# Kernel tuning notes

Hardware: AMD Instinct MI355X
Metric: run time of the kernel (lower is better)

Reference implementation:

```python
import jax, jax.numpy as jnp
import numpy as np

B, S, E = 1024, 128, 256   # batch, num fields, embed size
H, D = 8, 64               # head_num, att_embed_size
SCALING = False


def setup_inputs() -> dict:
    key = jax.random.key(0)
    k0, k1, k2, k3, k4 = jax.random.split(key, 5)
    return {
        "inputs": jax.random.normal(k0, (B, S, E), dtype=jnp.float32),
        "w_query": jax.random.truncated_normal(k1, -2.0, 2.0, (E, H * D), dtype=jnp.float32) * 0.05,
        "w_key": jax.random.truncated_normal(k2, -2.0, 2.0, (E, H * D), dtype=jnp.float32) * 0.05,
        "w_value": jax.random.truncated_normal(k3, -2.0, 2.0, (E, H * D), dtype=jnp.float32) * 0.05,
        "w_res": jax.random.truncated_normal(k4, -2.0, 2.0, (E, H * D), dtype=jnp.float32) * 0.05,
    }


def reference(inputs, w_query, w_key, w_value, w_res):
    b, s, _ = inputs.shape
    # QKV projections, split into heads: tf.split on last dim == reshape (b,s,H,D)
    q = (inputs @ w_query).reshape(b, s, H, D)
    k = (inputs @ w_key).reshape(b, s, H, D)
    v = (inputs @ w_value).reshape(b, s, H, D)
    scores = jnp.einsum("bqhd,bkhd->bhqk", q, k)
    if SCALING:
        scores = scores / jnp.sqrt(jnp.float32(D))
    att = jax.nn.softmax(scores, axis=-1)
    out = jnp.einsum("bhqk,bkhd->bqhd", att, v).reshape(b, s, H * D)
    out = out + inputs @ w_res  # residual projection (use_res=True)
    return jax.nn.relu(out)
```

## Files before the change

kernel.cpp:

```cpp
#include <hip/hip_runtime.h>

#define B_ 1024
#define S_ 128
#define E_ 256
#define H_ 8
#define D_ 64
#define HD_ 512

typedef short s16x8 __attribute__((ext_vector_type(8)));
typedef float f32x4 __attribute__((ext_vector_type(4)));
typedef unsigned int u32x4 __attribute__((ext_vector_type(4)));
typedef unsigned short u16;
typedef unsigned int u32;

struct U16x8 { u16 v[8]; };

__device__ __forceinline__ u16 f2bf(float f) {
  u32 u = __float_as_uint(f);
  u += 0x7FFFu + ((u >> 16) & 1u);
  return (u16)(u >> 16);
}

__device__ __forceinline__ u32 cvtpk_bf16(float lo, float hi) {
  u32 r;
  asm("v_cvt_pk_bf16_f32 %0, %1, %2" : "=v"(r) : "v"(lo), "v"(hi));
  return r;
}

__device__ __forceinline__ void dma_w(const u16* __restrict__ WF, int base8,
                                      u16* dst, int tid) {
  const char* g = (const char*)WF + (size_t)base8 * 32768 + (size_t)tid * 16;
  char* l = (char*)dst + tid * 16;
#pragma unroll
  for (int j = 0; j < 4; ++j)
    __builtin_amdgcn_global_load_lds(
        (const __attribute__((address_space(1))) void*)(g + j * 8192),
        (__attribute__((address_space(3))) void*)(l + j * 8192), 16, 0, 0);
}

__global__ __launch_bounds__(256) void probe_dtype(const u32* __restrict__ x,
                                                   u32* __restrict__ flag) {
  __shared__ int cnt;
  if (threadIdx.x == 0) cnt = 0;
  __syncthreads();
  u32 w = x[threadIdx.x];
  u32 e = (w >> 7) & 0xFFu;
  if (e > 96u && e < 160u) atomicAdd(&cnt, 1);
  __syncthreads();
  if (threadIdx.x == 0) flag[0] = (cnt > 128) ? 1u : 0u;
}

__global__ __launch_bounds__(256) void repack_w(
    const void* __restrict__ wqv, const void* __restrict__ wkv,
    const void* __restrict__ wvv, const void* __restrict__ wrv,
    const u32* __restrict__ flag, u16* __restrict__ wf) {
  bool isbf = (flag[0] != 0u);
  int t = blockIdx.x * 256 + threadIdx.x;
  int lane = t & 63;
  int tc   = (t >> 6) & 3;
  int ks   = (t >> 8) & 7;
  int h    = (t >> 11) & 7;
  int w    = (t >> 14) & 3;
  const void* srcv = (w == 0) ? wqv : (w == 1) ? wkv : (w == 2) ? wvv : wrv;
  int n  = h * D_ + tc * 16 + (lane & 15);
  int e0 = ks * 32 + (lane >> 4) * 8;
  U16x8 tmp;
  if (isbf) {
    const u16* s = (const u16*)srcv;
#pragma unroll
    for (int j = 0; j < 8; ++j) tmp.v[j] = s[(e0 + j) * HD_ + n];
  } else {
    const float* s = (const float*)srcv;
#pragma unroll
    for (int j = 0; j < 8; ++j) tmp.v[j] = f2bf(s[(e0 + j) * HD_ + n]);
  }
  *(u32x4*)(wf + (size_t)t * 8) = *(const u32x4*)tmp.v;
}

__device__ __forceinline__ void proj4_lds(const u16* __restrict__ Wb, int lane,
                                          const s16x8 xfrag[8], f32x4 acc[4]) {
  const u32x4* w4 = (const u32x4*)Wb + lane;
#pragma unroll
  for (int tc = 0; tc < 4; ++tc) acc[tc] = (f32x4){0.f, 0.f, 0.f, 0.f};
#pragma unroll
  for (int ks = 0; ks < 8; ++ks) {
#pragma unroll
    for (int tc = 0; tc < 4; ++tc) {
      u32x4 raw = w4[(ks * 4 + tc) * 64];
      s16x8 bfr = *(const s16x8*)&raw;
      acc[tc] = __builtin_amdgcn_mfma_f32_16x16x32_bf16(xfrag[ks], bfr, acc[tc], 0, 0, 0);
    }
  }
}

__device__ __forceinline__ void proj4_direct(const void* __restrict__ srcv, bool isbf,
                                             int h, int lane, const s16x8 xfrag[8],
                                             f32x4 acc[4]) {
#pragma unroll
  for (int tc = 0; tc < 4; ++tc) acc[tc] = (f32x4){0.f, 0.f, 0.f, 0.f};
  int e8 = (lane >> 4) * 8;
  int nc = h * D_ + (lane & 15);
#pragma unroll
  for (int ks = 0; ks < 8; ++ks) {
#pragma unroll
    for (int tc = 0; tc < 4; ++tc) {
      U16x8 tmp;
      if (isbf) {
        const u16* s = (const u16*)srcv;
#pragma unroll
        for (int j = 0; j < 8; ++j) tmp.v[j] = s[(ks * 32 + e8 + j) * HD_ + nc + tc * 16];
      } else {
        const float* s = (const float*)srcv;
#pragma unroll
        for (int j = 0; j < 8; ++j) tmp.v[j] = f2bf(s[(ks * 32 + e8 + j) * HD_ + nc + tc * 16]);
      }
      s16x8 bfr = *(const s16x8*)tmp.v;
      acc[tc] = __builtin_amdgcn_mfma_f32_16x16x32_bf16(xfrag[ks], bfr, acc[tc], 0, 0, 0);
    }
  }
}

__device__ __forceinline__ void scatter_qk(u16* dst, int w, int quad, int col,
                                           const f32x4 acc[4]) {
#pragma unroll
  for (int tc = 0; tc < 4; ++tc) {
    int ks2 = tc >> 1;
    int q2  = (tc & 1) * 2 + (col >> 3);
#pragma unroll
    for (int r = 0; r < 4; ++r)
      dst[(((w * 2 + ks2) * 64) + q2 * 16 + quad * 4 + r) * 8 + (col & 7)] =
          f2bf(acc[tc][r]);
  }
}

__device__ __forceinline__ void scatter_v(u16* Vf, int w, int quad, int col,
                                          const f32x4 acc[4]) {
#pragma unroll
  for (int tc = 0; tc < 4; ++tc)
#pragma unroll
    for (int r = 0; r < 4; ++r) {
      int srow = quad * 4 + r;
      int q2   = (w & 1) * 2 + (srow >> 3);
      Vf[((((w >> 1) * 4 + tc) * 64) + q2 * 16 + col) * 8 + (srow & 7)] =
          f2bf(acc[tc][r]);
    }
}

__global__ __launch_bounds__(512) void mha_fused(
    const void* __restrict__ Xv, const u16* __restrict__ WF,
    const void* __restrict__ wqv, const void* __restrict__ wkv,
    const void* __restrict__ wvv, const void* __restrict__ wrv,
    void* __restrict__ outv, const u32* __restrict__ flag, int useWF) {
  __shared__ __align__(16) u16 smem[73728];
  u16* Wb0 = smem;
  u16* Wb1 = smem + 16384;
  u16* Qf  = smem + 32768;
  u16* KfB = smem + 40960;
  u16* VfB = smem + 57344;

  const bool isbf = (flag[0] != 0u);
  const int tid  = threadIdx.x;
  const int w    = tid >> 6;
  const int lane = tid & 63;
  const int quad = lane >> 4;
  const int col  = lane & 15;
  const int b    = blockIdx.x;

  if (useWF) dma_w(WF, 0, Wb0, tid);

  s16x8 xfrag[8];
  {
    u32x4* xs = (u32x4*)KfB;
#pragma unroll
    for (int half = 0; half < 2; ++half) {
      int cbase = half * 2048;
#pragma unroll
      for (int k = 0; k < 4; ++k) {
        int c  = cbase + tid + k * 512;
        int s  = c >> 5;
        int e0 = (c & 31) * 8;
        U16x8 tmp;
        if (isbf) {
          const u32x4* xg = (const u32x4*)Xv + (size_t)b * 4096;
          u32x4 raw = xg[c];
          tmp = *(const U16x8*)&raw;
        } else {
          const f32x4* xg = (const f32x4*)Xv + (size_t)b * 8192;
          f32x4 lo = xg[2 * c], hi = xg[2 * c + 1];
#pragma unroll
          for (int j = 0; j < 4; ++j) { tmp.v[j] = f2bf(lo[j]); tmp.v[4 + j] = f2bf(hi[j]); }
        }
        xs[(((s >> 4) & 3) * 8 + (e0 >> 5)) * 64 + ((e0 >> 3) & 3) * 16 + (s & 15)] =
            *(const u32x4*)tmp.v;
      }
      __syncthreads();
      if ((w >> 2) == half) {
        int trl = w & 3;
#pragma unroll
        for (int ks = 0; ks < 8; ++ks) {
          u32x4 raw = xs[(trl * 8 + ks) * 64 + lane];
          xfrag[ks] = *(const s16x8*)&raw;
        }
      }
      __syncthreads();
    }
  }

  s16x8 aq[2];
  f32x4 ra[4];

  const int sl0 = (lane & 15) | ((lane & 16) << 1);
  const bool hiq = (lane >= 32);

  for (int h = 0; h <= H_; ++h) {
    const int hp = h - 1;
    const u16* Kp = KfB + (hp & 1) * 8192;
    const u16* Vp = VfB + (hp & 1) * 8192;
    u16* Kc = KfB + (h & 1) * 8192;
    u16* Vc = VfB + (h & 1) * 8192;

    f32x4 sacc[8];
    u32 wp[8][2];
    f32x4 oacc[4];
    float linv = 0.f;
    s16x8 aqn[2];
    f32x4 acc[4];

    __syncthreads();
    if (useWF && h < H_) dma_w(WF, 8 + h, Wb1, tid);
    if (h < H_) {
      if (useWF) proj4_lds(Wb0, lane, xfrag, acc);
      else       proj4_direct(wqv, isbf, h, lane, xfrag, acc);
      scatter_qk(Qf, w, quad, col, acc);
      aqn[0] = *(const s16x8*)(Qf + ((w * 2 + 0) * 64 + lane) * 8);
      aqn[1] = *(const s16x8*)(Qf + ((w * 2 + 1) * 64 + lane) * 8);
    }
    if (h > 0) {
#pragma unroll
      for (int tS = 0; tS < 8; ++tS) {
        sacc[tS] = (f32x4){0.f, 0.f, 0.f, 0.f};
#pragma unroll
        for (int k2 = 0; k2 < 2; ++k2) {
          s16x8 bk = *(const s16x8*)(Kp + ((tS * 2 + k2) * 64 + lane) * 8);
          sacc[tS] = __builtin_amdgcn_mfma_f32_16x16x32_bf16(bk, aq[k2], sacc[tS], 0, 0, 0);
        }
      }
    }
    if (h < H_) { aq[0] = aqn[0]; aq[1] = aqn[1]; }

    __syncthreads();
    if (useWF && h < H_) dma_w(WF, 16 + h, Wb0, tid);
    if (h < H_) {
      if (useWF) proj4_lds(Wb1, lane, xfrag, acc);
      else       proj4_direct(wkv, isbf, h, lane, xfrag, acc);
      scatter_qk(Kc, w, quad, col, acc);
    }
    if (h > 0) {
      float m = sacc[0][0];
#pragma unroll
      for (int tS = 0; tS < 8; ++tS)
#pragma unroll
        for (int r = 0; r < 4; ++r) m = fmaxf(m, sacc[tS][r]);
      m = fmaxf(m, __shfl_xor(m, 16));
      m = fmaxf(m, __shfl_xor(m, 32));
      float lsum = 0.f;
#pragma unroll
      for (int tS = 0; tS < 8; ++tS)
#pragma unroll
        for (int r = 0; r < 4; ++r) {
          float e = __expf(sacc[tS][r] - m);
          sacc[tS][r] = e;
          lsum += e;
        }
      lsum += __shfl_xor(lsum, 16);
      lsum += __shfl_xor(lsum, 32);
      linv = 1.0f / lsum;
#pragma unroll
      for (int tS = 0; tS < 8; ++tS) {
        wp[tS][0] = cvtpk_bf16(sacc[tS][0], sacc[tS][1]);
        wp[tS][1] = cvtpk_bf16(sacc[tS][2], sacc[tS][3]);
      }
    }

    __syncthreads();
    if (useWF && h < H_) dma_w(WF, 24 + h, Wb1, tid);
    if (h < H_) {
      if (useWF) proj4_lds(Wb0, lane, xfrag, acc);
      else       proj4_direct(wvv, isbf, h, lane, xfrag, acc);
      scatter_v(Vc, w, quad, col, acc);
    }
    if (h > 0) {
#pragma unroll
      for (int tc = 0; tc < 4; ++tc) oacc[tc] = (f32x4){0.f, 0.f, 0.f, 0.f};
#pragma unroll
      for (int kt = 0; kt < 4; ++kt) {
        int a00 = __shfl((int)wp[2 * kt][0],     sl0);
        int a01 = __shfl((int)wp[2 * kt][1],     sl0);
        int a10 = __shfl((int)wp[2 * kt + 1][0], sl0);
        int a11 = __shfl((int)wp[2 * kt + 1][1], sl0);
        int b00 = __shfl((int)wp[2 * kt][0],     sl0 + 16);
        int b01 = __shfl((int)wp[2 * kt][1],     sl0 + 16);
        int b10 = __shfl((int)wp[2 * kt + 1][0], sl0 + 16);
        int b11 = __shfl((int)wp[2 * kt + 1][1], sl0 + 16);
        u32x4 av;
        av[0] = (u32)(hiq ? a10 : a00);
        av[1] = (u32)(hiq ? a11 : a01);
        av[2] = (u32)(hiq ? b10 : b00);
        av[3] = (u32)(hiq ? b11 : b01);
        s16x8 ap = *(const s16x8*)&av;
#pragma unroll
        for (int tc = 0; tc < 4; ++tc) {
          s16x8 bv = *(const s16x8*)(Vp + ((kt * 4 + tc) * 64 + lane) * 8);
          oacc[tc] = __builtin_amdgcn_mfma_f32_16x16x32_bf16(ap, bv, oacc[tc], 0, 0, 0);
        }
      }
    }

    __syncthreads();
    if (useWF && h + 1 < H_) dma_w(WF, h + 1, Wb0, tid);
    if (h < H_) {
      if (useWF) proj4_lds(Wb1, lane, xfrag, acc);
      else       proj4_direct(wrv, isbf, h, lane, xfrag, acc);
    }
    if (h > 0) {
      float linv_e[4];
#pragma unroll
      for (int r = 0; r < 4; ++r) linv_e[r] = __shfl(linv, quad * 4 + r);
#pragma unroll
      for (int tc = 0; tc < 4; ++tc)
#pragma unroll
        for (int r = 0; r < 4; ++r) {
          float v = oacc[tc][r] * linv_e[r] + ra[tc][r];
          v = fmaxf(v, 0.f);
          int s = w * 16 + quad * 4 + r;
          size_t idx = ((size_t)b * S_ + s) * HD_ + hp * D_ + tc * 16 + col;
          if (isbf) ((u16*)outv)[idx] = f2bf(v);
          else      ((float*)outv)[idx] = v;
        }
    }
    if (h < H_) {
#pragma unroll
      for (int tc = 0; tc < 4; ++tc) ra[tc] = acc[tc];
    }
  }
}

extern "C" void kernel_launch(void* const* d_in, const int* in_sizes, int n_in,
                              void* d_out, int out_size, void* d_ws, size_t ws_size,
                              hipStream_t stream) {
  const void* X  = d_in[0];
  const void* wq = d_in[1];
  const void* wk = d_in[2];
  const void* wv = d_in[3];
  const void* wr = d_in[4];

  u32* flag = (u32*)d_ws;
  u16* wf   = (u16*)((char*)d_ws + 4096);
  int useWF = (ws_size >= (size_t)(1u << 20) + 4096) ? 1 : 0;

  probe_dtype<<<dim3(1), dim3(256), 0, stream>>>((const u32*)X, flag);
  if (useWF)
    repack_w<<<dim3(256), dim3(256), 0, stream>>>(wq, wk, wv, wr, flag, wf);
  mha_fused<<<dim3(B_), dim3(512), 0, stream>>>(X, wf, wq, wk, wv, wr, d_out, flag, useWF);
}
```

Baseline: 579.6 us.

## Process two batch elements per block to share staged weight tiles

Each block now handles two batch elements, so every weight tile copied into LDS feeds twice as many MFMAs, and the grid is halved. The head loop is rescheduled: the second batch's PV and epilogue are deferred to the next iteration, and the K/V buffers are split per batch instead of ping-ponged per head. The aim is to halve weight traffic into LDS and the per-block setup cost. In exchange, register pressure rises (two X fragment sets and two accumulator sets), which may cause spills. With fewer, longer blocks there is also less latitude to balance load across CUs.

```diff
diff --git a/kernel.cpp b/kernel.cpp
--- a/kernel.cpp
+++ b/kernel.cpp
@@ -77,18 +77,23 @@
   *(u32x4*)(wf + (size_t)t * 8) = *(const u32x4*)tmp.v;
 }
 
-__device__ __forceinline__ void proj4_lds(const u16* __restrict__ Wb, int lane,
-                                          const s16x8 xfrag[8], f32x4 acc[4]) {
+__device__ __forceinline__ void proj4_lds2(const u16* __restrict__ Wb, int lane,
+                                           const s16x8 xf0[8], const s16x8 xf1[8],
+                                           f32x4 a0[4], f32x4 a1[4]) {
   const u32x4* w4 = (const u32x4*)Wb + lane;
 #pragma unroll
-  for (int tc = 0; tc < 4; ++tc) acc[tc] = (f32x4){0.f, 0.f, 0.f, 0.f};
+  for (int tc = 0; tc < 4; ++tc) {
+    a0[tc] = (f32x4){0.f, 0.f, 0.f, 0.f};
+    a1[tc] = (f32x4){0.f, 0.f, 0.f, 0.f};
+  }
 #pragma unroll
   for (int ks = 0; ks < 8; ++ks) {
 #pragma unroll
     for (int tc = 0; tc < 4; ++tc) {
       u32x4 raw = w4[(ks * 4 + tc) * 64];
       s16x8 bfr = *(const s16x8*)&raw;
-      acc[tc] = __builtin_amdgcn_mfma_f32_16x16x32_bf16(xfrag[ks], bfr, acc[tc], 0, 0, 0);
+      a0[tc] = __builtin_amdgcn_mfma_f32_16x16x32_bf16(xf0[ks], bfr, a0[tc], 0, 0, 0);
+      a1[tc] = __builtin_amdgcn_mfma_f32_16x16x32_bf16(xf1[ks], bfr, a1[tc], 0, 0, 0);
     }
   }
 }
@@ -144,6 +149,129 @@
       Vf[((((w >> 1) * 4 + tc) * 64) + q2 * 16 + col) * 8 + (srow & 7)] =
           f2bf(acc[tc][r]);
     }
+}
+
+__device__ __forceinline__ void qk_sm(const u16* __restrict__ Kp, const s16x8 aqb[2],
+                                      int lane, u32 wp[8][2], float& linv) {
+  f32x4 sacc[8];
+#pragma unroll
+  for (int tS = 0; tS < 8; ++tS) {
+    sacc[tS] = (f32x4){0.f, 0.f, 0.f, 0.f};
+#pragma unroll
+    for (int k2 = 0; k2 < 2; ++k2) {
+      s16x8 bk = *(const s16x8*)(Kp + ((tS * 2 + k2) * 64 + lane) * 8);
+      sacc[tS] = __builtin_amdgcn_mfma_f32_16x16x32_bf16(bk, aqb[k2], sacc[tS], 0, 0, 0);
+    }
+  }
+  float m = sacc[0][0];
+#pragma unroll
+  for (int tS = 0; tS < 8; ++tS)
+#pragma unroll
+    for (int r = 0; r < 4; ++r) m = fmaxf(m, sacc[tS][r]);
+  m = fmaxf(m, __shfl_xor(m, 16));
+  m = fmaxf(m, __shfl_xor(m, 32));
+  float lsum = 0.f;
+#pragma unroll
+  for (int tS = 0; tS < 8; ++tS)
+#pragma unroll
+    for (int r = 0; r < 4; ++r) {
+      float e = __expf(sacc[tS][r] - m);
+      sacc[tS][r] = e;
+      lsum += e;
+    }
+  lsum += __shfl_xor(lsum, 16);
+  lsum += __shfl_xor(lsum, 32);
+  linv = 1.0f / lsum;
+#pragma unroll
+  for (int tS = 0; tS < 8; ++tS) {
+    wp[tS][0] = cvtpk_bf16(sacc[tS][0], sacc[tS][1]);
+    wp[tS][1] = cvtpk_bf16(sacc[tS][2], sacc[tS][3]);
+  }
+}
+
+__device__ __forceinline__ void pv_epi(const u16* __restrict__ Vp, const u32 wp[8][2],
+                                       float linv, const f32x4 ra[4],
+                                       void* __restrict__ outv, bool isbf, int bb,
+                                       int hh, int w, int lane, int quad, int col,
+                                       int sl0, bool hiq) {
+  f32x4 oacc[4];
+#pragma unroll
+  for (int tc = 0; tc < 4; ++tc) oacc[tc] = (f32x4){0.f, 0.f, 0.f, 0.f};
+#pragma unroll
+  for (int kt = 0; kt < 4; ++kt) {
+    int a00 = __shfl((int)wp[2 * kt][0],     sl0);
+    int a01 = __shfl((int)wp[2 * kt][1],     sl0);
+    int a10 = __shfl((int)wp[2 * kt + 1][0], sl0);
+    int a11 = __shfl((int)wp[2 * kt + 1][1], sl0);
+    int b00 = __shfl((int)wp[2 * kt][0],     sl0 + 16);
+    int b01 = __shfl((int)wp[2 * kt][1],     sl0 + 16);
+    int b10 = __shfl((int)wp[2 * kt + 1][0], sl0 + 16);
+    int b11 = __shfl((int)wp[2 * kt + 1][1], sl0 + 16);
+    u32x4 av;
+    av[0] = (u32)(hiq ? a10 : a00);
+    av[1] = (u32)(hiq ? a11 : a01);
+    av[2] = (u32)(hiq ? b10 : b00);
+    av[3] = (u32)(hiq ? b11 : b01);
+    s16x8 ap = *(const s16x8*)&av;
+#pragma unroll
+    for (int tc = 0; tc < 4; ++tc) {
+      s16x8 bv = *(const s16x8*)(Vp + ((kt * 4 + tc) * 64 + lane) * 8);
+      oacc[tc] = __builtin_amdgcn_mfma_f32_16x16x32_bf16(ap, bv, oacc[tc], 0, 0, 0);
+    }
+  }
+  float linv_e[4];
+#pragma unroll
+  for (int r = 0; r < 4; ++r) linv_e[r] = __shfl(linv, quad * 4 + r);
+#pragma unroll
+  for (int tc = 0; tc < 4; ++tc)
+#pragma unroll
+    for (int r = 0; r < 4; ++r) {
+      float v = oacc[tc][r] * linv_e[r] + ra[tc][r];
+      v = fmaxf(v, 0.f);
+      int s = w * 16 + quad * 4 + r;
+      size_t idx = ((size_t)bb * S_ + s) * HD_ + hh * D_ + tc * 16 + col;
+      if (isbf) ((u16*)outv)[idx] = f2bf(v);
+      else      ((float*)outv)[idx] = v;
+    }
+}
+
+__device__ __forceinline__ void stage_x(const void* __restrict__ Xv, bool isbf, int bb,
+                                        int tid, int w, int lane, u16* scratch,
+                                        s16x8 xfrag[8]) {
+  u32x4* xs = (u32x4*)scratch;
+#pragma unroll
+  for (int half = 0; half < 2; ++half) {
+    int cbase = half * 2048;
+#pragma unroll
+    for (int k = 0; k < 4; ++k) {
+      int c  = cbase + tid + k * 512;
+      int s  = c >> 5;
+      int e0 = (c & 31) * 8;
+      U16x8 tmp;
+      if (isbf) {
+        const u32x4* xg = (const u32x4*)Xv + (size_t)bb * 4096;
+        u32x4 raw = xg[c];
+        tmp = *(const U16x8*)&raw;
+      } else {
+        const f32x4* xg = (const f32x4*)Xv + (size_t)bb * 8192;
+        f32x4 lo = xg[2 * c], hi = xg[2 * c + 1];
+#pragma unroll
+        for (int j = 0; j < 4; ++j) { tmp.v[j] = f2bf(lo[j]); tmp.v[4 + j] = f2bf(hi[j]); }
+      }
+      xs[(((s >> 4) & 3) * 8 + (e0 >> 5)) * 64 + ((e0 >> 3) & 3) * 16 + (s & 15)] =
+          *(const u32x4*)tmp.v;
+    }
+    __syncthreads();
+    if ((w >> 2) == half) {
+      int trl = w & 3;
+#pragma unroll
+      for (int ks = 0; ks < 8; ++ks) {
+        u32x4 raw = xs[(trl * 8 + ks) * 64 + lane];
+        xfrag[ks] = *(const s16x8*)&raw;
+      }
+    }
+    __syncthreads();
+  }
 }
 
 __global__ __launch_bounds__(512) void mha_fused(
@@ -155,8 +283,10 @@
   u16* Wb0 = smem;
   u16* Wb1 = smem + 16384;
   u16* Qf  = smem + 32768;
-  u16* KfB = smem + 40960;
-  u16* VfB = smem + 57344;
+  u16* Kb0 = smem + 40960;
+  u16* Kb1 = smem + 49152;
+  u16* Vb0 = smem + 57344;
+  u16* Vb1 = smem + 65536;
 
   const bool isbf = (flag[0] != 0u);
   const int tid  = threadIdx.x;
@@ -164,184 +294,76 @@
   const int lane = tid & 63;
   const int quad = lane >> 4;
   const int col  = lane & 15;
-  const int b    = blockIdx.x;
+  const int b0i  = blockIdx.x * 2;
+  const int b1i  = b0i + 1;
 
   if (useWF) dma_w(WF, 0, Wb0, tid);
 
-  s16x8 xfrag[8];
-  {
-    u32x4* xs = (u32x4*)KfB;
-#pragma unroll
-    for (int half = 0; half < 2; ++half) {
-      int cbase = half * 2048;
-#pragma unroll
-      for (int k = 0; k < 4; ++k) {
-        int c  = cbase + tid + k * 512;
-        int s  = c >> 5;
-        int e0 = (c & 31) * 8;
-        U16x8 tmp;
-        if (isbf) {
-          const u32x4* xg = (const u32x4*)Xv + (size_t)b * 4096;
-          u32x4 raw = xg[c];
-          tmp = *(const U16x8*)&raw;
-        } else {
-          const f32x4* xg = (const f32x4*)Xv + (size_t)b * 8192;
-          f32x4 lo = xg[2 * c], hi = xg[2 * c + 1];
-#pragma unroll
-          for (int j = 0; j < 4; ++j) { tmp.v[j] = f2bf(lo[j]); tmp.v[4 + j] = f2bf(hi[j]); }
-        }
-        xs[(((s >> 4) & 3) * 8 + (e0 >> 5)) * 64 + ((e0 >> 3) & 3) * 16 + (s & 15)] =
-            *(const u32x4*)tmp.v;
-      }
-      __syncthreads();
-      if ((w >> 2) == half) {
-        int trl = w & 3;
-#pragma unroll
-        for (int ks = 0; ks < 8; ++ks) {
-          u32x4 raw = xs[(trl * 8 + ks) * 64 + lane];
-          xfrag[ks] = *(const s16x8*)&raw;
-        }
-      }
-      __syncthreads();
-    }
-  }
-
-  s16x8 aq[2];
-  f32x4 ra[4];
+  s16x8 xf0[8], xf1[8];
+  stage_x(Xv, isbf, b0i, tid, w, lane, Kb0, xf0);
+  stage_x(Xv, isbf, b1i, tid, w, lane, Kb0, xf1);
 
   const int sl0 = (lane & 15) | ((lane & 16) << 1);
   const bool hiq = (lane >= 32);
 
+  u32 wp1[8][2];
+  float linv1 = 0.f;
+  f32x4 ra1[4];
+
   for (int h = 0; h <= H_; ++h) {
-    const int hp = h - 1;
-    const u16* Kp = KfB + (hp & 1) * 8192;
-    const u16* Vp = VfB + (hp & 1) * 8192;
-    u16* Kc = KfB + (h & 1) * 8192;
-    u16* Vc = VfB + (h & 1) * 8192;
-
-    f32x4 sacc[8];
-    u32 wp[8][2];
-    f32x4 oacc[4];
-    float linv = 0.f;
-    s16x8 aqn[2];
-    f32x4 acc[4];
+    s16x8 aq0[2], aq1[2];
 
     __syncthreads();
     if (useWF && h < H_) dma_w(WF, 8 + h, Wb1, tid);
-    if (h < H_) {
-      if (useWF) proj4_lds(Wb0, lane, xfrag, acc);
-      else       proj4_direct(wqv, isbf, h, lane, xfrag, acc);
-      scatter_qk(Qf, w, quad, col, acc);
-      aqn[0] = *(const s16x8*)(Qf + ((w * 2 + 0) * 64 + lane) * 8);
-      aqn[1] = *(const s16x8*)(Qf + ((w * 2 + 1) * 64 + lane) * 8);
-    }
-    if (h > 0) {
-#pragma unroll
-      for (int tS = 0; tS < 8; ++tS) {
-        sacc[tS] = (f32x4){0.f, 0.f, 0.f, 0.f};
-#pragma unroll
-        for (int k2 = 0; k2 < 2; ++k2) {
-          s16x8 bk = *(const s16x8*)(Kp + ((tS * 2 + k2) * 64 + lane) * 8);
-          sacc[tS] = __builtin_amdgcn_mfma_f32_16x16x32_bf16(bk, aq[k2], sacc[tS], 0, 0, 0);
-        }
-      }
-    }
-    if (h < H_) { aq[0] = aqn[0]; aq[1] = aqn[1]; }
-
-    __syncthreads();
-    if (useWF && h < H_) dma_w(WF, 16 + h, Wb0, tid);
-    if (h < H_) {
-      if (useWF) proj4_lds(Wb1, lane, xfrag, acc);
-      else       proj4_direct(wkv, isbf, h, lane, xfrag, acc);
-      scatter_qk(Kc, w, quad, col, acc);
-    }
-    if (h > 0) {
-      float m = sacc[0][0];
-#pragma unroll
-      for (int tS = 0; tS < 8; ++tS)
-#pragma unroll
-        for (int r = 0; r < 4; ++r) m = fmaxf(m, sacc[tS][r]);
-      m = fmaxf(m, __shfl_xor(m, 16));
-      m = fmaxf(m, __shfl_xor(m, 32));
-      float lsum = 0.f;
-#pragma unroll
-      for (int tS = 0; tS < 8; ++tS)
-#pragma unroll
-        for (int r = 0; r < 4; ++r) {
-          float e = __expf(sacc[tS][r] - m);
-          sacc[tS][r] = e;
-          lsum += e;
-        }
-      lsum += __shfl_xor(lsum, 16);
-      lsum += __shfl_xor(lsum, 32);
-      linv = 1.0f / lsum;
-#pragma unroll
-      for (int tS = 0; tS < 8; ++tS) {
-        wp[tS][0] = cvtpk_bf16(sacc[tS][0], sacc[tS][1]);
-        wp[tS][1] = cvtpk_bf16(sacc[tS][2], sacc[tS][3]);
-      }
-    }
-
-    __syncthreads();
-    if (useWF && h < H_) dma_w(WF, 24 + h, Wb1, tid);
-    if (h < H_) {
-      if (useWF) proj4_lds(Wb0, lane, xfrag, acc);
-      else       proj4_direct(wvv, isbf, h, lane, xfrag, acc);
-      scatter_v(Vc, w, quad, col, acc);
-    }
-    if (h > 0) {
-#pragma unroll
-      for (int tc = 0; tc < 4; ++tc) oacc[tc] = (f32x4){0.f, 0.f, 0.f, 0.f};
-#pragma unroll
-      for (int kt = 0; kt < 4; ++kt) {
-        int a00 = __shfl((int)wp[2 * kt][0],     sl0);
-        int a01 = __shfl((int)wp[2 * kt][1],     sl0);
-        int a10 = __shfl((int)wp[2 * kt + 1][0], sl0);
-        int a11 = __shfl((int)wp[2 * kt + 1][1], sl0);
-        int b00 = __shfl((int)wp[2 * kt][0],     sl0 + 16);
-        int b01 = __shfl((int)wp[2 * kt][1],     sl0 + 16);
-        int b10 = __shfl((int)wp[2 * kt + 1][0], sl0 + 16);
-        int b11 = __shfl((int)wp[2 * kt + 1][1], sl0 + 16);
-        u32x4 av;
-        av[0] = (u32)(hiq ? a10 : a00);
-        av[1] = (u32)(hiq ? a11 : a01);
-        av[2] = (u32)(hiq ? b10 : b00);
-        av[3] = (u32)(hiq ? b11 : b01);
-        s16x8 ap = *(const s16x8*)&av;
-#pragma unroll
-        for (int tc = 0; tc < 4; ++tc) {
-          s16x8 bv = *(const s16x8*)(Vp + ((kt * 4 + tc) * 64 + lane) * 8);
-          oacc[tc] = __builtin_amdgcn_mfma_f32_16x16x32_bf16(ap, bv, oacc[tc], 0, 0, 0);
-        }
-      }
-    }
+    if (h > 0)
+      pv_epi(Vb1, wp1, linv1, ra1, outv, isbf, b1i, h - 1, w, lane, quad, col, sl0, hiq);
+    if (h == H_) break;
+    {
+      f32x4 a0[4], a1[4];
+      if (useWF) proj4_lds2(Wb0, lane, xf0, xf1, a0, a1);
+      else { proj4_direct(wqv, isbf, h, lane, xf0, a0);
+             proj4_direct(wqv, isbf, h, lane, xf1, a1); }
+      scatter_qk(Qf, w, quad, col, a0);
+      aq0[0] = *(const s16x8*)(Qf + ((w * 2 + 0) * 64 + lane) * 8);
+      aq0[1] = *(const s16x8*)(Qf + ((w * 2 + 1) * 64 + lane) * 8);
+      scatter_qk(Qf, w, quad, col, a1);
+      aq1[0] = *(const s16x8*)(Qf + ((w * 2 + 0) * 64 + lane) * 8);
+      aq1[1] = *(const s16x8*)(Qf + ((w * 2 + 1) * 64 + lane) * 8);
+    }
+
+    __syncthreads();
+    if (useWF) dma_w(WF, 16 + h, Wb0, tid);
+    {
+      f32x4 a0[4], a1[4];
+      if (useWF) proj4_lds2(Wb1, lane, xf0, xf1, a0, a1);
+      else { proj4_direct(wkv, isbf, h, lane, xf0, a0);
+             proj4_direct(wkv, isbf, h, lane, xf1, a1); }
+      scatter_qk(Kb0, w, quad, col, a0);
+      scatter_qk(Kb1, w, quad, col, a1);
+    }
+
+    __syncthreads();
+    if (useWF) dma_w(WF, 24 + h, Wb1, tid);
+    u32 wp0[8][2];
+    float linv0 = 0.f;
+    {
+      f32x4 a0[4], a1[4];
+      if (useWF) proj4_lds2(Wb0, lane, xf0, xf1, a0, a1);
+      else { proj4_direct(wvv, isbf, h, lane, xf0, a0);
+             proj4_direct(wvv, isbf, h, lane, xf1, a1); }
+      scatter_v(Vb0, w, quad, col, a0);
+      scatter_v(Vb1, w, quad, col, a1);
+    }
+    qk_sm(Kb0, aq0, lane, wp0, linv0);
 
     __syncthreads();
     if (useWF && h + 1 < H_) dma_w(WF, h + 1, Wb0, tid);
-    if (h < H_) {
-      if (useWF) proj4_lds(Wb1, lane, xfrag, acc);
-      else       proj4_direct(wrv, isbf, h, lane, xfrag, acc);
-    }
-    if (h > 0) {
-      float linv_e[4];
-#pragma unroll
-      for (int r = 0; r < 4; ++r) linv_e[r] = __shfl(linv, quad * 4 + r);
-#pragma unroll
-      for (int tc = 0; tc < 4; ++tc)
-#pragma unroll
-        for (int r = 0; r < 4; ++r) {
-          float v = oacc[tc][r] * linv_e[r] + ra[tc][r];
-          v = fmaxf(v, 0.f);
-          int s = w * 16 + quad * 4 + r;
-          size_t idx = ((size_t)b * S_ + s) * HD_ + hp * D_ + tc * 16 + col;
-          if (isbf) ((u16*)outv)[idx] = f2bf(v);
-          else      ((float*)outv)[idx] = v;
-        }
-    }
-    if (h < H_) {
-#pragma unroll
-      for (int tc = 0; tc < 4; ++tc) ra[tc] = acc[tc];
-    }
+    f32x4 ra0[4];
+    if (useWF) proj4_lds2(Wb1, lane, xf0, xf1, ra0, ra1);
+    else { proj4_direct(wrv, isbf, h, lane, xf0, ra0);
+           proj4_direct(wrv, isbf, h, lane, xf1, ra1); }
+    qk_sm(Kb1, aq1, lane, wp1, linv1);
+    pv_epi(Vb0, wp0, linv0, ra0, outv, isbf, b0i, h, w, lane, quad, col, sl0, hiq);
   }
 }
 
@@ -361,5 +383,5 @@
   probe_dtype<<<dim3(1), dim3(256), 0, stream>>>((const u32*)X, flag);
   if (useWF)
     repack_w<<<dim3(256), dim3(256), 0, stream>>>(wq, wk, wv, wr, flag, wf);
-  mha_fused<<<dim3(B_), dim3(512), 0, stream>>>(X, wf, wq, wk, wv, wr, d_out, flag, useWF);
-}
+  mha_fused<<<dim3(B_ / 2), dim3(512), 0, stream>>>(X, wf, wq, wk, wv, wr, d_out, flag, useWF);
+}
```

Result: slower. 798.1 us (+37.7%).
